# Kernel optimization log

Hardware: AMD Instinct MI355X
Metric: run time of the kernel (lower is better)

The kernel has to match this reference:

```python
import jax, jax.numpy as jnp
import numpy as np
from jax import lax

T, L, K = 1024, 32, 128
BEG = 0  # index of '[BEG]' in the label dict


def setup_inputs() -> dict:
    key = jax.random.key(0)
    kx, kw, kl = jax.random.split(key, 3)
    X = jax.random.normal(kx, (T, L, L, K), dtype=jnp.float32)
    w = jax.random.normal(kw, (K,), dtype=jnp.float32)  # nn.Parameter, init N(0,1)
    label = jax.random.randint(kl, (T,), 0, L, dtype=jnp.int32)
    return {"X": X, "w": w, "label": label}


def reference(X, w, label):
    """CRF negative log-likelihood (forward algorithm over log-potential matrices)."""
    # Ms[t, i, j] = log-potential of transition i->j at step t  (X @ w)
    Ms = jnp.einsum('tijk,k->tij', X, w)  # [T, L, L]

    # forward recurrence: alpha_t[j] = logsumexp_i(alpha_{t-1}[i] + Ms[t, i, j])
    alpha0 = Ms[0, BEG, :]  # [L]

    def step(alpha, M):
        new = jax.nn.logsumexp(alpha[:, None] + M, axis=0)
        return new, None

    alpha_last, _ = lax.scan(step, alpha0, Ms[1:])
    logZ = jax.nn.logsumexp(alpha_last)

    # gold-path score: sum_t Ms[t, prev_label_t, label_t], prev_0 = BEG
    prev = jnp.concatenate([jnp.array([BEG], dtype=label.dtype), label[:-1]])
    t_idx = jnp.arange(Ms.shape[0])
    path_score = jnp.sum(Ms[t_idx, prev, label])

    return -path_score + logZ
```

## Files before the change

kernel.cpp:

```cpp
#include <hip/hip_runtime.h>

#define LL 32
#define LDP 33
#define TT 1024

#define MS_OFF 0
#define P0_OFF (MS_OFF + TT * 1024)
#define P1_OFF (P0_OFF + 128 * 1024)

__device__ __forceinline__ float lse_mul_step(float a, const float* Bcol) {
  float s[LL];
  #pragma unroll
  for (int k = 0; k < LL; k++) s[k] = __shfl(a, k, 32) + Bcol[k * LDP];
  float t[16];
  #pragma unroll
  for (int k = 0; k < 16; k++) t[k] = fmaxf(s[k], s[k + 16]);
  #pragma unroll
  for (int st = 8; st >= 1; st >>= 1) {
    #pragma unroll
    for (int k = 0; k < st; k++) t[k] = fmaxf(t[k], t[k + st]);
  }
  const float mx = t[0];
  float a0 = 0.f, a1 = 0.f, a2 = 0.f, a3 = 0.f;
  #pragma unroll
  for (int k = 0; k < LL; k += 4) {
    a0 += __expf(s[k]     - mx);
    a1 += __expf(s[k + 1] - mx);
    a2 += __expf(s[k + 2] - mx);
    a3 += __expf(s[k + 3] - mx);
  }
  return mx + __logf((a0 + a1) + (a2 + a3));
}

__global__ __launch_bounds__(256, 4) void crf_gemv(
    const float4* __restrict__ X4, const float* __restrict__ w,
    float* __restrict__ ms) {
  __shared__ float sm[512];
  const int tid = threadIdx.x;
  const int wv = tid >> 6;
  const int l  = tid & 63;
  const int r8 = l >> 3;
  const int l8 = l & 7;
  float4 wq[4];
  #pragma unroll
  for (int i = 0; i < 4; i++)
    wq[i] = reinterpret_cast<const float4*>(w)[i * 8 + l8];
  const size_t rowbase = (size_t)blockIdx.x * 512;
  const float4* xp = X4 + rowbase * 32;

  #pragma unroll 2
  for (int it = 0; it < 16; it++) {
    const int row = it * 32 + wv * 8 + r8;
    const float4* rp = xp + (size_t)row * 32;
    float acc = 0.f;
    #pragma unroll
    for (int i = 0; i < 4; i++) {
      const float4 xv = rp[i * 8 + l8];
      acc = fmaf(xv.x, wq[i].x, acc);
      acc = fmaf(xv.y, wq[i].y, acc);
      acc = fmaf(xv.z, wq[i].z, acc);
      acc = fmaf(xv.w, wq[i].w, acc);
    }
    acc += __shfl_xor(acc, 1);
    acc += __shfl_xor(acc, 2);
    acc += __shfl_xor(acc, 4);
    if (l8 == 0) sm[row] = acc;
  }
  __syncthreads();
  if (tid < 128)
    reinterpret_cast<float4*>(ms + rowbase)[tid] =
        reinterpret_cast<const float4*>(sm)[tid];
}

__global__ __launch_bounds__(1024, 1) void crf_leaf8(
    const float* __restrict__ ms, float* __restrict__ p0) {
  __shared__ float S[8][LL][LDP];
  const int blk = blockIdx.x, tid = threadIdx.x;
  const int i = tid >> 5, j = tid & 31;
  #pragma unroll
  for (int m = 0; m < 8; m++) S[m][i][j] = ms[((size_t)blk * 8 + m) * 1024 + tid];
  __syncthreads();
  float a = (blk == 0) ? ((i == j) ? 0.f : -1e30f) : S[0][i][j];
  #pragma unroll
  for (int m = 1; m < 8; m++) a = lse_mul_step(a, &S[m][0][j]);
  p0[(size_t)blk * 1024 + tid] = a;
}

__global__ __launch_bounds__(1024, 1) void crf_comb16(
    const float* __restrict__ src, float* __restrict__ dst) {
  __shared__ float S[16][LL][LDP];
  const int blk = blockIdx.x, tid = threadIdx.x;
  const int i = tid >> 5, j = tid & 31;
  #pragma unroll
  for (int m = 0; m < 16; m++)
    S[m][i][j] = src[((size_t)blk * 16 + m) * 1024 + tid];
  __syncthreads();
  float a = S[0][i][j];
  #pragma unroll
  for (int m = 1; m < 16; m++) a = lse_mul_step(a, &S[m][0][j]);
  dst[(size_t)blk * 1024 + tid] = a;
}

__global__ __launch_bounds__(1024, 1) void crf_final(
    const float* __restrict__ ws, const int* __restrict__ label,
    float* __restrict__ out) {
  __shared__ float S[8][LL][LDP];
  __shared__ float redm[16], reds[16], redp[16];
  const int tid = threadIdx.x, i = tid >> 5, j = tid & 31;
  #pragma unroll
  for (int m = 0; m < 8; m++) S[m][i][j] = ws[P1_OFF + m * 1024 + tid];
  __syncthreads();
  float a = S[0][i][j];
  #pragma unroll
  for (int m = 1; m < 8; m++) a = lse_mul_step(a, &S[m][0][j]);
  const float v = ws[MS_OFF + i] + a;
  const int lab = label[tid];
  const int pv = (tid == 0) ? 0 : label[tid - 1];
  const float pval = ws[MS_OFF + (size_t)tid * 1024 + pv * 32 + lab];
  float mx = v;
  #pragma unroll
  for (int o = 32; o >= 1; o >>= 1) mx = fmaxf(mx, __shfl_xor(mx, o));
  const int wid = tid >> 6, lane = tid & 63;
  if (lane == 0) redm[wid] = mx;
  __syncthreads();
  float mb = redm[0];
  #pragma unroll
  for (int q = 1; q < 16; q++) mb = fmaxf(mb, redm[q]);
  float e = __expf(v - mb);
  float p = pval;
  #pragma unroll
  for (int o = 32; o >= 1; o >>= 1) {
    e += __shfl_xor(e, o);
    p += __shfl_xor(p, o);
  }
  if (lane == 0) { reds[wid] = e; redp[wid] = p; }
  __syncthreads();
  if (tid == 0) {
    float s = 0.f, ps = 0.f;
    for (int q = 0; q < 16; q++) { s += reds[q]; ps += redp[q]; }
    out[0] = -ps + (mb + __logf(s));
  }
}

extern "C" void kernel_launch(void* const* d_in, const int* in_sizes, int n_in,
                              void* d_out, int out_size, void* d_ws, size_t ws_size,
                              hipStream_t stream) {
  const float4* X4 = (const float4*)d_in[0];
  const float* w = (const float*)d_in[1];
  const int* label = (const int*)d_in[2];
  float* out = (float*)d_out;
  float* ws = (float*)d_ws;

  crf_gemv<<<2048, 256, 0, stream>>>(X4, w, ws + MS_OFF);
  crf_leaf8<<<128, 1024, 0, stream>>>(ws + MS_OFF, ws + P0_OFF);
  crf_comb16<<<8, 1024, 0, stream>>>(ws + P0_OFF, ws + P1_OFF);
  crf_final<<<1, 1024, 0, stream>>>(ws, label, out);
}
```

Before: 162.8 us.

## Use tree-reduced log-semiring matrix products and LDS-staged direct loads in GEMV

The sequential chains of log-semiring matrix-vector steps in the leaf, combine and final kernels are replaced by a balanced binary tree of 32x32 log-semiring matrix products per block, with each level reducing eight matrices. This shortens the serial dependency depth per kernel, at the cost of an extra combine launch. The GEMV now uses 1024 blocks that stage 16 KB tiles into LDS with global_load_lds, and the launch bound rises to six blocks per SM. The GEMV change adds two barriers per tile and drops the final vectorized store.

```diff
diff --git a/kernel.cpp b/kernel.cpp
--- a/kernel.cpp
+++ b/kernel.cpp
@@ -1,17 +1,19 @@
 #include <hip/hip_runtime.h>
 
 #define LL 32
-#define LDP 33
 #define TT 1024
 
 #define MS_OFF 0
-#define P0_OFF (MS_OFF + TT * 1024)
-#define P1_OFF (P0_OFF + 128 * 1024)
+#define Q1_OFF (MS_OFF + 1024 * 1024)
+#define Q2_OFF (Q1_OFF + 128 * 1024)
+#define Q3_OFF (Q2_OFF + 16 * 1024)
 
-__device__ __forceinline__ float lse_mul_step(float a, const float* Bcol) {
+__device__ __forceinline__ float lse_cell(const float A[LL][LL + 1],
+                                          const float B[LL][LL + 1],
+                                          int i, int j) {
   float s[LL];
   #pragma unroll
-  for (int k = 0; k < LL; k++) s[k] = __shfl(a, k, 32) + Bcol[k * LDP];
+  for (int k = 0; k < LL; k++) s[k] = A[i][k] + B[k][j];
   float t[16];
   #pragma unroll
   for (int k = 0; k < 16; k++) t[k] = fmaxf(s[k], s[k + 16]);
@@ -32,96 +34,89 @@
   return mx + __logf((a0 + a1) + (a2 + a3));
 }
 
-__global__ __launch_bounds__(256, 4) void crf_gemv(
-    const float4* __restrict__ X4, const float* __restrict__ w,
+__global__ __launch_bounds__(256, 6) void crf_gemv(
+    const float* __restrict__ X, const float* __restrict__ w,
     float* __restrict__ ms) {
-  __shared__ float sm[512];
+  __shared__ float buf[4096];
   const int tid = threadIdx.x;
-  const int wv = tid >> 6;
-  const int l  = tid & 63;
-  const int r8 = l >> 3;
-  const int l8 = l & 7;
-  float4 wq[4];
+  const int lane = tid & 63, wid = tid >> 6;
+  const int c = tid >> 3, sub = tid & 7;
+  float4 wr[4];
   #pragma unroll
-  for (int i = 0; i < 4; i++)
-    wq[i] = reinterpret_cast<const float4*>(w)[i * 8 + l8];
-  const size_t rowbase = (size_t)blockIdx.x * 512;
-  const float4* xp = X4 + rowbase * 32;
+  for (int s = 0; s < 4; s++)
+    wr[s] = reinterpret_cast<const float4*>(w)[sub * 4 + s];
+  const char* xb = (const char*)X + (size_t)blockIdx.x * 524288;
+  float* msb = ms + (size_t)blockIdx.x * 1024;
 
-  #pragma unroll 2
-  for (int it = 0; it < 16; it++) {
-    const int row = it * 32 + wv * 8 + r8;
-    const float4* rp = xp + (size_t)row * 32;
+  for (int tile = 0; tile < 32; tile++) {
+    const char* src = xb + tile * 16384 + wid * 4096 + lane * 16;
+    #pragma unroll
+    for (int u = 0; u < 4; u++) {
+      __builtin_amdgcn_global_load_lds(
+          (const __attribute__((address_space(1))) void*)(src + u * 1024),
+          (__attribute__((address_space(3))) void*)&buf[(wid * 4 + u) * 256],
+          16, 0, 0);
+    }
+    __syncthreads();
+    const float4* bf = reinterpret_cast<const float4*>(buf);
     float acc = 0.f;
     #pragma unroll
-    for (int i = 0; i < 4; i++) {
-      const float4 xv = rp[i * 8 + l8];
-      acc = fmaf(xv.x, wq[i].x, acc);
-      acc = fmaf(xv.y, wq[i].y, acc);
-      acc = fmaf(xv.z, wq[i].z, acc);
-      acc = fmaf(xv.w, wq[i].w, acc);
+    for (int s = 0; s < 4; s++) {
+      const float4 xv = bf[c * 32 + sub * 4 + s];
+      acc = fmaf(xv.x, wr[s].x,
+            fmaf(xv.y, wr[s].y, fmaf(xv.z, wr[s].z, fmaf(xv.w, wr[s].w, acc))));
     }
     acc += __shfl_xor(acc, 1);
     acc += __shfl_xor(acc, 2);
     acc += __shfl_xor(acc, 4);
-    if (l8 == 0) sm[row] = acc;
+    if (sub == 0) msb[tile * 32 + c] = acc;
+    __syncthreads();
   }
-  __syncthreads();
-  if (tid < 128)
-    reinterpret_cast<float4*>(ms + rowbase)[tid] =
-        reinterpret_cast<const float4*>(sm)[tid];
 }
 
-__global__ __launch_bounds__(1024, 1) void crf_leaf8(
-    const float* __restrict__ ms, float* __restrict__ p0) {
-  __shared__ float S[8][LL][LDP];
+__global__ __launch_bounds__(1024, 1) void crf_comb8(
+    const float* __restrict__ src, float* __restrict__ dst, int skip0) {
+  __shared__ float S[8][LL][LL + 1];
+  __shared__ float PQ[4][LL][LL + 1];
   const int blk = blockIdx.x, tid = threadIdx.x;
   const int i = tid >> 5, j = tid & 31;
   #pragma unroll
-  for (int m = 0; m < 8; m++) S[m][i][j] = ms[((size_t)blk * 8 + m) * 1024 + tid];
+  for (int m = 0; m < 8; m++) {
+    float v = src[((size_t)blk * 8 + m) * 1024 + tid];
+    if (skip0 && blk == 0 && m == 0) v = (i == j) ? 0.f : -1e30f;
+    S[m][i][j] = v;
+  }
   __syncthreads();
-  float a = (blk == 0) ? ((i == j) ? 0.f : -1e30f) : S[0][i][j];
   #pragma unroll
-  for (int m = 1; m < 8; m++) a = lse_mul_step(a, &S[m][0][j]);
-  p0[(size_t)blk * 1024 + tid] = a;
+  for (int q = 0; q < 4; q++)
+    PQ[q][i][j] = lse_cell(S[2 * q], S[2 * q + 1], i, j);
+  __syncthreads();
+  S[0][i][j] = lse_cell(PQ[0], PQ[1], i, j);
+  S[1][i][j] = lse_cell(PQ[2], PQ[3], i, j);
+  __syncthreads();
+  dst[(size_t)blk * 1024 + tid] = lse_cell(S[0], S[1], i, j);
 }
 
-__global__ __launch_bounds__(1024, 1) void crf_comb16(
-    const float* __restrict__ src, float* __restrict__ dst) {
-  __shared__ float S[16][LL][LDP];
-  const int blk = blockIdx.x, tid = threadIdx.x;
-  const int i = tid >> 5, j = tid & 31;
-  #pragma unroll
-  for (int m = 0; m < 16; m++)
-    S[m][i][j] = src[((size_t)blk * 16 + m) * 1024 + tid];
-  __syncthreads();
-  float a = S[0][i][j];
-  #pragma unroll
-  for (int m = 1; m < 16; m++) a = lse_mul_step(a, &S[m][0][j]);
-  dst[(size_t)blk * 1024 + tid] = a;
-}
-
-__global__ __launch_bounds__(1024, 1) void crf_final(
+__global__ __launch_bounds__(1024, 1) void crf_final2(
     const float* __restrict__ ws, const int* __restrict__ label,
     float* __restrict__ out) {
-  __shared__ float S[8][LL][LDP];
+  __shared__ float S[2][LL][LL + 1];
   __shared__ float redm[16], reds[16], redp[16];
   const int tid = threadIdx.x, i = tid >> 5, j = tid & 31;
   #pragma unroll
-  for (int m = 0; m < 8; m++) S[m][i][j] = ws[P1_OFF + m * 1024 + tid];
+  for (int m = 0; m < 2; m++) S[m][i][j] = ws[Q3_OFF + m * 1024 + tid];
   __syncthreads();
-  float a = S[0][i][j];
-  #pragma unroll
-  for (int m = 1; m < 8; m++) a = lse_mul_step(a, &S[m][0][j]);
+  const float a = lse_cell(S[0], S[1], i, j);
   const float v = ws[MS_OFF + i] + a;
   const int lab = label[tid];
   const int pv = (tid == 0) ? 0 : label[tid - 1];
   const float pval = ws[MS_OFF + (size_t)tid * 1024 + pv * 32 + lab];
+
   float mx = v;
   #pragma unroll
   for (int o = 32; o >= 1; o >>= 1) mx = fmaxf(mx, __shfl_xor(mx, o));
-  const int wid = tid >> 6, lane = tid & 63;
-  if (lane == 0) redm[wid] = mx;
+  const int wv = tid >> 6, lane = tid & 63;
+  if (lane == 0) redm[wv] = mx;
   __syncthreads();
   float mb = redm[0];
   #pragma unroll
@@ -133,7 +128,7 @@
     e += __shfl_xor(e, o);
     p += __shfl_xor(p, o);
   }
-  if (lane == 0) { reds[wid] = e; redp[wid] = p; }
+  if (lane == 0) { reds[wv] = e; redp[wv] = p; }
   __syncthreads();
   if (tid == 0) {
     float s = 0.f, ps = 0.f;
@@ -145,14 +140,15 @@
 extern "C" void kernel_launch(void* const* d_in, const int* in_sizes, int n_in,
                               void* d_out, int out_size, void* d_ws, size_t ws_size,
                               hipStream_t stream) {
-  const float4* X4 = (const float4*)d_in[0];
+  const float* X = (const float*)d_in[0];
   const float* w = (const float*)d_in[1];
   const int* label = (const int*)d_in[2];
   float* out = (float*)d_out;
   float* ws = (float*)d_ws;
 
-  crf_gemv<<<2048, 256, 0, stream>>>(X4, w, ws + MS_OFF);
-  crf_leaf8<<<128, 1024, 0, stream>>>(ws + MS_OFF, ws + P0_OFF);
-  crf_comb16<<<8, 1024, 0, stream>>>(ws + P0_OFF, ws + P1_OFF);
-  crf_final<<<1, 1024, 0, stream>>>(ws, label, out);
+  crf_gemv<<<1024, 256, 0, stream>>>(X, w, ws + MS_OFF);
+  crf_comb8<<<128, 1024, 0, stream>>>(ws + MS_OFF, ws + Q1_OFF, 1);
+  crf_comb8<<<16, 1024, 0, stream>>>(ws + Q1_OFF, ws + Q2_OFF, 0);
+  crf_comb8<<<2, 1024, 0, stream>>>(ws + Q2_OFF, ws + Q3_OFF, 0);
+  crf_final2<<<1, 1024, 0, stream>>>(ws, label, out);
 }
```

After: 156.2 us. 4.1% less time.
